# Performance work log

Measured on AMD Instinct MI355X. Metric: run time of the kernel, lower is better.

## Reference

```python
import jax, jax.numpy as jnp
import numpy as np

D = 128        # num_hidden
NIN = 384      # num_in (edge feature dim)
FF = 4 * D     # dense inner dim
SCALE = 30.0
EPS = 1e-5     # haiku LayerNorm default

gelu = lambda x: jax.nn.gelu(x, approximate=False)

def _ln(x, g, o):
    mu = jnp.mean(x, axis=-1, keepdims=True)
    var = jnp.var(x, axis=-1, keepdims=True)
    return (x - mu) * jax.lax.rsqrt(var + EPS) * g + o

def setup_inputs() -> dict:
    key = jax.random.key(0)
    ks = jax.random.split(key, 12)
    B, N, K = 4, 2048, 48
    s = lambda fan_in: 1.0 / np.sqrt(fan_in)
    return {
        "h_V": jax.random.normal(ks[0], (B, N, D), jnp.float32),
        "h_E": jax.random.normal(ks[1], (B, N, K, NIN), jnp.float32),
        "mask_V": jnp.ones((B, N), jnp.float32),
        "mask_attend": jnp.ones((B, N, K), jnp.float32),
        "W1": jax.random.normal(ks[2], (D + NIN, D), jnp.float32) * s(D + NIN),
        "b1": jnp.zeros((D,), jnp.float32),
        "W2": jax.random.normal(ks[3], (D, D), jnp.float32) * s(D),
        "b2": jnp.zeros((D,), jnp.float32),
        "W3": jax.random.normal(ks[4], (D, D), jnp.float32) * s(D),
        "b3": jnp.zeros((D,), jnp.float32),
        "W_in": jax.random.normal(ks[5], (D, FF), jnp.float32) * s(D),
        "b_in": jnp.zeros((FF,), jnp.float32),
        "W_out": jax.random.normal(ks[6], (FF, D), jnp.float32) * s(FF),
        "b_out": jnp.zeros((D,), jnp.float32),
        "g1": jnp.ones((D,), jnp.float32),
        "o1": jnp.zeros((D,), jnp.float32),
        "g2": jnp.ones((D,), jnp.float32),
        "o2": jnp.zeros((D,), jnp.float32),
    }

def reference(h_V, h_E, mask_V, mask_attend, W1, b1, W2, b2, W3, b3,
              W_in, b_in, W_out, b_out, g1, o1, g2, o2):
    B, N, K, _ = h_E.shape
    # broadcast node feats over neighbors and concat with edge feats: (B,N,K,D+NIN)
    h_V_exp = jnp.broadcast_to(h_V[:, :, None, :], (B, N, K, h_V.shape[-1]))
    h_EV = jnp.concatenate([h_V_exp, h_E], axis=-1)
    h = gelu(h_EV @ W1 + b1)
    h = gelu(h @ W2 + b2)
    h_message = h @ W3 + b3                      # (B,N,K,D)
    h_message = mask_attend[..., None] * h_message
    dh = jnp.sum(h_message, axis=-2) / SCALE      # (B,N,D)
    h_V = _ln(h_V + dh, g1, o1)                   # dropout rate=0 -> identity
    dh = gelu(h_V @ W_in + b_in) @ W_out + b_out  # position-wise FFN
    h_V = _ln(h_V + dh, g2, o2)
    h_V = mask_V[..., None] * h_V
    return h_V
```

## Files before the change

### kernel.cpp

```cpp
#include <hip/hip_runtime.h>
#include <hip/hip_bf16.h>

typedef unsigned short u16;
typedef __attribute__((ext_vector_type(8))) short short8;
typedef __attribute__((ext_vector_type(4))) float f32x4;

#define SD   128
#define SNIN 384
#define SK   48
#define HPAD 136
#define FPAD 520

#define OFF_W1A   0
#define OFF_W1B   32768
#define OFF_W2    131072
#define OFF_W3    163840
#define OFF_WIN   196608
#define OFF_WOUT  327680

__device__ __forceinline__ u16 f2b(float f){
  union { float f; unsigned u; } v; v.f = f;
  unsigned r = (v.u + 0x7FFFu + ((v.u >> 16) & 1u)) >> 16;
  return (u16)r;
}
__device__ __forceinline__ short8 ldg8(const u16* p){
  return *reinterpret_cast<const short8*>(p);
}
__device__ __forceinline__ short8 cvt8(const float* p){
  float4 a = *reinterpret_cast<const float4*>(p);
  float4 b = *reinterpret_cast<const float4*>(p + 4);
  short8 r;
  r[0]=(short)f2b(a.x); r[1]=(short)f2b(a.y); r[2]=(short)f2b(a.z); r[3]=(short)f2b(a.w);
  r[4]=(short)f2b(b.x); r[5]=(short)f2b(b.y); r[6]=(short)f2b(b.z); r[7]=(short)f2b(b.w);
  return r;
}

__device__ __forceinline__ float gelu_f(float x){
  float xc = fminf(3.0f, fmaxf(-3.0f, x));
  float u  = xc*xc;
  float p  = fmaf(u, fmaf(u, fmaf(u, -4.81034e-4f, 1.185750e-2f), -1.1877797e-1f), 7.9165011e-1f);
  float t  = xc*p;
  float hx = 0.5f*x;
  return fmaf(t, hx, hx);
}

__global__ __launch_bounds__(256) void prep_pack(
    const float* __restrict__ W1, const float* __restrict__ W2, const float* __restrict__ W3,
    const float* __restrict__ Win, const float* __restrict__ Wout, u16* __restrict__ ws)
{
  int t = blockIdx.x*256 + threadIdx.x;
  const float* src; int stride, rowoff, NT; u16* dst; int local;
  if (t < 2048)       { src=W1;  stride=SD;  rowoff=0;   NT=8;  dst=ws+OFF_W1A/2;  local=t;       }
  else if (t < 8192)  { src=W1;  stride=SD;  rowoff=128; NT=8;  dst=ws+OFF_W1B/2;  local=t-2048;  }
  else if (t < 10240) { src=W2;  stride=SD;  rowoff=0;   NT=8;  dst=ws+OFF_W2/2;   local=t-8192;  }
  else if (t < 12288) { src=W3;  stride=SD;  rowoff=0;   NT=8;  dst=ws+OFF_W3/2;   local=t-10240; }
  else if (t < 20480) { src=Win; stride=512; rowoff=0;   NT=32; dst=ws+OFF_WIN/2;  local=t-12288; }
  else                { src=Wout;stride=SD;  rowoff=0;   NT=8;  dst=ws+OFF_WOUT/2; local=t-20480; }
  int lane = local & 63;
  int blk  = local >> 6;
  int nt = blk % NT, ks = blk / NT;
  int k0 = rowoff + ks*32 + (lane>>4)*8;
  int n  = nt*16 + (lane & 15);
  union { u16 a[8]; short8 v; } tmp;
  #pragma unroll
  for (int j=0;j<8;j++) tmp.a[j] = f2b(src[(size_t)(k0+j)*stride + n]);
  *reinterpret_cast<short8*>(dst + (size_t)local*8) = tmp.v;
}

__global__ __launch_bounds__(256, 2) void dec_nodes(
    const float* __restrict__ hV, const float* __restrict__ hE, const float* __restrict__ mAtt,
    const float* __restrict__ b1, const float* __restrict__ b2, const float* __restrict__ b3,
    const float* __restrict__ g1, const float* __restrict__ o1,
    const u16* __restrict__ ws, float* __restrict__ u_out)
{
  __shared__ u16 HH[4][SK*HPAD];

  const int tid  = threadIdx.x;
  const int w    = tid >> 6;
  const int lane = tid & 63;
  const int quad = lane >> 4;
  const int l16  = lane & 15;
  const int g    = blockIdx.x*4 + w;
  u16* HHw = HH[w];

  float base1v[8];
  {
    f32x4 accb[8];
    #pragma unroll
    for (int nt=0;nt<8;nt++) accb[nt] = (f32x4){0.f,0.f,0.f,0.f};
    const u16* Bb = ws + OFF_W1A/2 + (size_t)lane*8;
    #pragma unroll
    for (int ks=0; ks<4; ks++){
      short8 af = cvt8(hV + (size_t)g*SD + ks*32 + quad*8);
      #pragma unroll
      for (int nt=0; nt<8; nt++){
        short8 bf = ldg8(Bb + ((size_t)(ks*8+nt)*64)*8);
        accb[nt] = __builtin_amdgcn_mfma_f32_16x16x32_bf16(af, bf, accb[nt], 0,0,0);
      }
    }
    #pragma unroll
    for (int nt=0;nt<8;nt++) base1v[nt] = accb[nt][0] + b1[nt*16 + l16];
  }

  f32x4 acc[24];
  #pragma unroll
  for (int i=0;i<24;i++) acc[i] = (f32x4){0.f,0.f,0.f,0.f};
  {
    const float* Ab = hE + (size_t)g*(SK*SNIN) + (size_t)l16*SNIN + quad*8;
    const u16*  Bb = ws + OFF_W1B/2 + (size_t)lane*8;
    #pragma unroll
    for (int ks=0; ks<12; ks++){
      short8 af[3];
      #pragma unroll
      for (int mt=0; mt<3; mt++) af[mt] = cvt8(Ab + (size_t)mt*16*SNIN + ks*32);
      #pragma unroll
      for (int nt=0; nt<8; nt++){
        short8 bf = ldg8(Bb + ((size_t)(ks*8+nt)*64)*8);
        #pragma unroll
        for (int mt=0; mt<3; mt++)
          acc[mt*8+nt] = __builtin_amdgcn_mfma_f32_16x16x32_bf16(af[mt], bf, acc[mt*8+nt], 0,0,0);
      }
    }
    #pragma unroll
    for (int mt=0; mt<3; mt++)
      #pragma unroll
      for (int nt=0; nt<8; nt++)
        #pragma unroll
        for (int i=0;i<4;i++){
          int row = mt*16 + quad*4 + i;
          HHw[row*HPAD + nt*16 + l16] = f2b(gelu_f(acc[mt*8+nt][i] + base1v[nt]));
        }
  }
  __syncthreads();

  #pragma unroll
  for (int i=0;i<24;i++) acc[i] = (f32x4){0.f,0.f,0.f,0.f};
  {
    const u16* Bb = ws + OFF_W2/2 + (size_t)lane*8;
    #pragma unroll
    for (int ks=0; ks<4; ks++){
      short8 af[3];
      #pragma unroll
      for (int mt=0; mt<3; mt++)
        af[mt] = *reinterpret_cast<const short8*>(&HHw[(mt*16+l16)*HPAD + ks*32 + quad*8]);
      #pragma unroll
      for (int nt=0; nt<8; nt++){
        short8 bf = ldg8(Bb + ((size_t)(ks*8+nt)*64)*8);
        #pragma unroll
        for (int mt=0; mt<3; mt++)
          acc[mt*8+nt] = __builtin_amdgcn_mfma_f32_16x16x32_bf16(af[mt], bf, acc[mt*8+nt], 0,0,0);
      }
    }
  }
  __syncthreads();
  {
    #pragma unroll
    for (int mt=0; mt<3; mt++)
      #pragma unroll
      for (int nt=0; nt<8; nt++){
        float bb = b2[nt*16 + l16];
        #pragma unroll
        for (int i=0;i<4;i++){
          int row = mt*16 + quad*4 + i;
          HHw[row*HPAD + nt*16 + l16] = f2b(gelu_f(acc[mt*8+nt][i] + bb));
        }
      }
  }
  __syncthreads();

  #pragma unroll
  for (int i=0;i<24;i++) acc[i] = (f32x4){0.f,0.f,0.f,0.f};
  {
    const u16* Bb = ws + OFF_W3/2 + (size_t)lane*8;
    #pragma unroll
    for (int ks=0; ks<4; ks++){
      short8 af[3];
      #pragma unroll
      for (int mt=0; mt<3; mt++)
        af[mt] = *reinterpret_cast<const short8*>(&HHw[(mt*16+l16)*HPAD + ks*32 + quad*8]);
      #pragma unroll
      for (int nt=0; nt<8; nt++){
        short8 bf = ldg8(Bb + ((size_t)(ks*8+nt)*64)*8);
        #pragma unroll
        for (int mt=0; mt<3; mt++)
          acc[mt*8+nt] = __builtin_amdgcn_mfma_f32_16x16x32_bf16(af[mt], bf, acc[mt*8+nt], 0,0,0);
      }
    }
  }
  float p[8];
  {
    #pragma unroll
    for (int nt=0;nt<8;nt++) p[nt] = 0.f;
    #pragma unroll
    for (int mt=0; mt<3; mt++)
      #pragma unroll
      for (int i=0;i<4;i++){
        float m = mAtt[(size_t)g*SK + mt*16 + quad*4 + i];
        #pragma unroll
        for (int nt=0; nt<8; nt++){
          float bb = b3[nt*16 + l16];
          p[nt] = fmaf(m, acc[mt*8+nt][i] + bb, p[nt]);
        }
      }
    #pragma unroll
    for (int nt=0;nt<8;nt++){
      p[nt] += __shfl_down(p[nt], 32, 64);
      p[nt] += __shfl_down(p[nt], 16, 64);
      p[nt]  = __shfl(p[nt], l16, 64);
    }
  }

  {
    float x[8];
    float s = 0.f, q = 0.f;
    #pragma unroll
    for (int nt=0;nt<8;nt++){
      x[nt] = hV[(size_t)g*SD + nt*16 + l16] + p[nt]*(1.0f/30.0f);
      s += x[nt]; q = fmaf(x[nt], x[nt], q);
    }
    #pragma unroll
    for (int off=1; off<64; off<<=1){ s += __shfl_xor(s, off, 64); q += __shfl_xor(q, off, 64); }
    float mu  = s * (1.0f/512.0f);
    float var = q * (1.0f/512.0f) - mu*mu;
    float rs  = rsqrtf(var + 1e-5f);
    #pragma unroll
    for (int k=0;k<2;k++){
      int nt = 2*quad + k;
      float uv = (x[nt]-mu)*rs*g1[nt*16+l16] + o1[nt*16+l16];
      u_out[(size_t)g*SD + nt*16 + l16] = uv;
    }
  }
}

__global__ __launch_bounds__(128) void ffn_ln(
    const float* __restrict__ b_in, const float* __restrict__ b_out,
    const float* __restrict__ g2, const float* __restrict__ o2, const float* __restrict__ mV,
    const u16* __restrict__ ws, float* __restrict__ uo)
{
  __shared__ u16 fS[2][16*FPAD];
  const int tid = threadIdx.x, w = tid>>6, lane = tid&63, quad = lane>>4, l16 = lane&15;
  const int m0 = blockIdx.x*32 + w*16;

  short8 afr[4];
  const float* Ap = uo + (size_t)(m0 + l16)*SD + quad*8;
  #pragma unroll
  for (int ks=0; ks<4; ks++) afr[ks] = cvt8(Ap + ks*32);

  #pragma unroll
  for (int nb=0; nb<4; nb++){
    f32x4 acc[8];
    #pragma unroll
    for (int t=0;t<8;t++) acc[t] = (f32x4){0.f,0.f,0.f,0.f};
    const u16* Bp = ws + OFF_WIN/2 + ((size_t)(nb*8)*64 + lane)*8;
    #pragma unroll
    for (int ks=0; ks<4; ks++){
      #pragma unroll
      for (int t=0;t<8;t++){
        short8 bf = ldg8(Bp + ((size_t)ks*32 + t)*512);
        acc[t] = __builtin_amdgcn_mfma_f32_16x16x32_bf16(afr[ks], bf, acc[t], 0,0,0);
      }
    }
    #pragma unroll
    for (int t=0;t<8;t++){
      int coln = nb*128 + t*16 + l16;
      float bi = b_in[coln];
      #pragma unroll
      for (int i=0;i<4;i++)
        fS[w][(quad*4+i)*FPAD + coln] = f2b(gelu_f(acc[t][i] + bi));
    }
  }
  __syncthreads();

  f32x4 acc2[8];
  #pragma unroll
  for (int t=0;t<8;t++) acc2[t] = (f32x4){0.f,0.f,0.f,0.f};
  const u16* Bo = ws + OFF_WOUT/2 + (size_t)lane*8;
  #pragma unroll
  for (int ks=0; ks<16; ks++){
    const short8 af = *reinterpret_cast<const short8*>(&fS[w][l16*FPAD + ks*32 + quad*8]);
    #pragma unroll
    for (int t=0;t<8;t++){
      short8 bf = ldg8(Bo + ((size_t)ks*8 + t)*512);
      acc2[t] = __builtin_amdgcn_mfma_f32_16x16x32_bf16(af, bf, acc2[t], 0,0,0);
    }
  }

  float bov[8], g2v[8], o2v[8];
  #pragma unroll
  for (int t=0;t<8;t++){
    int cl = t*16 + l16;
    bov[t] = b_out[cl]; g2v[t] = g2[cl]; o2v[t] = o2[cl];
  }
  #pragma unroll
  for (int i=0;i<4;i++){
    int r = m0 + quad*4 + i;
    float xv[8];
    float s = 0.f, q = 0.f;
    #pragma unroll
    for (int t=0;t<8;t++){
      xv[t] = uo[(size_t)r*SD + t*16 + l16] + acc2[t][i] + bov[t];
      s += xv[t]; q = fmaf(xv[t], xv[t], q);
    }
    #pragma unroll
    for (int mk=1; mk<16; mk<<=1){ s += __shfl_xor(s, mk, 64); q += __shfl_xor(q, mk, 64); }
    float mu  = s * (1.0f/128.0f);
    float var = q * (1.0f/128.0f) - mu*mu;
    float rs  = rsqrtf(var + 1e-5f);
    float mv  = mV[r];
    #pragma unroll
    for (int t=0;t<8;t++)
      uo[(size_t)r*SD + t*16 + l16] = mv * ((xv[t]-mu)*rs*g2v[t] + o2v[t]);
  }
}

extern "C" void kernel_launch(void* const* d_in, const int* in_sizes, int n_in,
                              void* d_out, int out_size, void* d_ws, size_t ws_size,
                              hipStream_t stream) {
  (void)n_in; (void)out_size; (void)ws_size;
  const float* hV    = (const float*)d_in[0];
  const float* hE    = (const float*)d_in[1];
  const float* mV    = (const float*)d_in[2];
  const float* mAtt  = (const float*)d_in[3];
  const float* W1    = (const float*)d_in[4];
  const float* b1    = (const float*)d_in[5];
  const float* W2    = (const float*)d_in[6];
  const float* b2    = (const float*)d_in[7];
  const float* W3    = (const float*)d_in[8];
  const float* b3    = (const float*)d_in[9];
  const float* Win   = (const float*)d_in[10];
  const float* b_in  = (const float*)d_in[11];
  const float* Wout  = (const float*)d_in[12];
  const float* b_out = (const float*)d_in[13];
  const float* g1    = (const float*)d_in[14];
  const float* o1    = (const float*)d_in[15];
  const float* g2    = (const float*)d_in[16];
  const float* o2    = (const float*)d_in[17];
  u16*   ws   = (u16*)d_ws;
  float* outp = (float*)d_out;
  const int NG = in_sizes[0] / SD;

  hipLaunchKernelGGL(prep_pack, dim3(112), dim3(256), 0, stream, W1, W2, W3, Win, Wout, ws);
  hipLaunchKernelGGL(dec_nodes, dim3(NG/4), dim3(256), 0, stream,
                     hV, hE, mAtt, b1, b2, b3, g1, o1, ws, outp);
  hipLaunchKernelGGL(ffn_ln, dim3(NG/32), dim3(128), 0, stream,
                     b_in, b_out, g2, o2, mV, ws, outp);
}
```

Before: 1.005 ms.

## Prefetch hE and weight fragments, use hardware bf16 pack, re-split FFN across waves

Replaces the software bf16 rounding with v_cvt_pk_bf16_f32 inline asm. It software-pipelines the first edge GEMM by loading hE tiles two k-steps ahead in rotating register buffers, and double-buffers weight fragments in the 128x128 GEMMs. The FFN kernel is restructured so four waves share 16 rows, splitting the hidden and output columns across waves and staging through shared memory. The aim is to hide global load latency on the hE stream and raise FFN parallelism, at the cost of more registers, which could cut occupancy under the (256,2) launch bounds.

```diff
diff --git a/kernel.cpp b/kernel.cpp
--- a/kernel.cpp
+++ b/kernel.cpp
@@ -26,13 +26,18 @@
 __device__ __forceinline__ short8 ldg8(const u16* p){
   return *reinterpret_cast<const short8*>(p);
 }
+__device__ __forceinline__ short8 pack8(float4 a, float4 b){
+  union { unsigned u[4]; short8 s; } r;
+  asm("v_cvt_pk_bf16_f32 %0, %1, %2" : "=v"(r.u[0]) : "v"(a.x), "v"(a.y));
+  asm("v_cvt_pk_bf16_f32 %0, %1, %2" : "=v"(r.u[1]) : "v"(a.z), "v"(a.w));
+  asm("v_cvt_pk_bf16_f32 %0, %1, %2" : "=v"(r.u[2]) : "v"(b.x), "v"(b.y));
+  asm("v_cvt_pk_bf16_f32 %0, %1, %2" : "=v"(r.u[3]) : "v"(b.z), "v"(b.w));
+  return r.s;
+}
 __device__ __forceinline__ short8 cvt8(const float* p){
   float4 a = *reinterpret_cast<const float4*>(p);
   float4 b = *reinterpret_cast<const float4*>(p + 4);
-  short8 r;
-  r[0]=(short)f2b(a.x); r[1]=(short)f2b(a.y); r[2]=(short)f2b(a.z); r[3]=(short)f2b(a.w);
-  r[4]=(short)f2b(b.x); r[5]=(short)f2b(b.y); r[6]=(short)f2b(b.z); r[7]=(short)f2b(b.w);
-  return r;
+  return pack8(a, b);
 }
 
 __device__ __forceinline__ float gelu_f(float x){
@@ -67,6 +72,55 @@
   *reinterpret_cast<short8*>(dst + (size_t)local*8) = tmp.v;
 }
 
+__device__ __forceinline__ void mlp128(const u16* __restrict__ Bb, const u16* HHw,
+                                       int l16, int quad, f32x4 acc[24])
+{
+  short8 bc[8], bn[8];
+  #pragma unroll
+  for (int nt=0;nt<8;nt++) bc[nt] = ldg8(Bb + ((size_t)nt*64)*8);
+  #pragma unroll
+  for (int ks=0; ks<4; ks++){
+    if (ks < 3){
+      #pragma unroll
+      for (int nt=0;nt<8;nt++) bn[nt] = ldg8(Bb + ((size_t)((ks+1)*8+nt)*64)*8);
+    }
+    short8 af[3];
+    #pragma unroll
+    for (int mt=0; mt<3; mt++)
+      af[mt] = *reinterpret_cast<const short8*>(&HHw[(size_t)(mt*16+l16)*HPAD + ks*32 + quad*8]);
+    #pragma unroll
+    for (int nt=0; nt<8; nt++)
+      #pragma unroll
+      for (int mt=0; mt<3; mt++)
+        acc[mt*8+nt] = __builtin_amdgcn_mfma_f32_16x16x32_bf16(af[mt], bc[nt], acc[mt*8+nt], 0,0,0);
+    if (ks < 3){
+      #pragma unroll
+      for (int nt=0;nt<8;nt++) bc[nt] = bn[nt];
+    }
+  }
+}
+
+#define LDA(BUF, kk) { _Pragma("unroll") for (int mt=0; mt<3; mt++){ \
+    BUF[mt][0] = *reinterpret_cast<const float4*>(Ab + (size_t)mt*16*SNIN + (kk)*32); \
+    BUF[mt][1] = *reinterpret_cast<const float4*>(Ab + (size_t)mt*16*SNIN + (kk)*32 + 4); } }
+
+#define G1STEP(CUR, NXT, ks, PF) { \
+    if (PF) LDA(NXT, (ks)+2); \
+    short8 af[3]; \
+    _Pragma("unroll") for (int mt=0; mt<3; mt++) af[mt] = pack8(CUR[mt][0], CUR[mt][1]); \
+    _Pragma("unroll") for (int nt=0; nt<8; nt++){ \
+      short8 bf = ldg8(Bb + ((size_t)((ks)*8+nt)*64)*8); \
+      _Pragma("unroll") for (int mt=0; mt<3; mt++) \
+        acc[mt*8+nt] = __builtin_amdgcn_mfma_f32_16x16x32_bf16(af[mt], bf, acc[mt*8+nt], 0,0,0); \
+    } }
+
+#define B1STEP(HB, ks) { \
+    short8 af = pack8(HB[0], HB[1]); \
+    _Pragma("unroll") for (int nt=0; nt<8; nt++){ \
+      short8 bf = ldg8(Bb1 + ((size_t)((ks)*8+nt)*64)*8); \
+      accb[nt] = __builtin_amdgcn_mfma_f32_16x16x32_bf16(af, bf, accb[nt], 0,0,0); \
+    } }
+
 __global__ __launch_bounds__(256, 2) void dec_nodes(
     const float* __restrict__ hV, const float* __restrict__ hE, const float* __restrict__ mAtt,
     const float* __restrict__ b1, const float* __restrict__ b2, const float* __restrict__ b3,
@@ -88,16 +142,14 @@
     f32x4 accb[8];
     #pragma unroll
     for (int nt=0;nt<8;nt++) accb[nt] = (f32x4){0.f,0.f,0.f,0.f};
-    const u16* Bb = ws + OFF_W1A/2 + (size_t)lane*8;
-    #pragma unroll
-    for (int ks=0; ks<4; ks++){
-      short8 af = cvt8(hV + (size_t)g*SD + ks*32 + quad*8);
-      #pragma unroll
-      for (int nt=0; nt<8; nt++){
-        short8 bf = ldg8(Bb + ((size_t)(ks*8+nt)*64)*8);
-        accb[nt] = __builtin_amdgcn_mfma_f32_16x16x32_bf16(af, bf, accb[nt], 0,0,0);
-      }
-    }
+    const u16* Bb1 = ws + OFF_W1A/2 + (size_t)lane*8;
+    const float* hp = hV + (size_t)g*SD + quad*8;
+    float4 H0[2], H1[2], H2[2], H3[2];
+    H0[0] = *reinterpret_cast<const float4*>(hp);       H0[1] = *reinterpret_cast<const float4*>(hp+4);
+    H1[0] = *reinterpret_cast<const float4*>(hp+32);    H1[1] = *reinterpret_cast<const float4*>(hp+36);
+    H2[0] = *reinterpret_cast<const float4*>(hp+64);    H2[1] = *reinterpret_cast<const float4*>(hp+68);
+    H3[0] = *reinterpret_cast<const float4*>(hp+96);    H3[1] = *reinterpret_cast<const float4*>(hp+100);
+    B1STEP(H0,0); B1STEP(H1,1); B1STEP(H2,2); B1STEP(H3,3);
     #pragma unroll
     for (int nt=0;nt<8;nt++) base1v[nt] = accb[nt][0] + b1[nt*16 + l16];
   }
@@ -108,19 +160,12 @@
   {
     const float* Ab = hE + (size_t)g*(SK*SNIN) + (size_t)l16*SNIN + quad*8;
     const u16*  Bb = ws + OFF_W1B/2 + (size_t)lane*8;
-    #pragma unroll
-    for (int ks=0; ks<12; ks++){
-      short8 af[3];
-      #pragma unroll
-      for (int mt=0; mt<3; mt++) af[mt] = cvt8(Ab + (size_t)mt*16*SNIN + ks*32);
-      #pragma unroll
-      for (int nt=0; nt<8; nt++){
-        short8 bf = ldg8(Bb + ((size_t)(ks*8+nt)*64)*8);
-        #pragma unroll
-        for (int mt=0; mt<3; mt++)
-          acc[mt*8+nt] = __builtin_amdgcn_mfma_f32_16x16x32_bf16(af[mt], bf, acc[mt*8+nt], 0,0,0);
-      }
-    }
+    float4 A0[3][2], A1[3][2], A2[3][2];
+    LDA(A0,0); LDA(A1,1);
+    G1STEP(A0,A2,0,1);  G1STEP(A1,A0,1,1);  G1STEP(A2,A1,2,1);
+    G1STEP(A0,A2,3,1);  G1STEP(A1,A0,4,1);  G1STEP(A2,A1,5,1);
+    G1STEP(A0,A2,6,1);  G1STEP(A1,A0,7,1);  G1STEP(A2,A1,8,1);
+    G1STEP(A0,A2,9,1);  G1STEP(A1,A0,10,0); G1STEP(A2,A1,11,0);
     #pragma unroll
     for (int mt=0; mt<3; mt++)
       #pragma unroll
@@ -135,23 +180,7 @@
 
   #pragma unroll
   for (int i=0;i<24;i++) acc[i] = (f32x4){0.f,0.f,0.f,0.f};
-  {
-    const u16* Bb = ws + OFF_W2/2 + (size_t)lane*8;
-    #pragma unroll
-    for (int ks=0; ks<4; ks++){
-      short8 af[3];
-      #pragma unroll
-      for (int mt=0; mt<3; mt++)
-        af[mt] = *reinterpret_cast<const short8*>(&HHw[(mt*16+l16)*HPAD + ks*32 + quad*8]);
-      #pragma unroll
-      for (int nt=0; nt<8; nt++){
-        short8 bf = ldg8(Bb + ((size_t)(ks*8+nt)*64)*8);
-        #pragma unroll
-        for (int mt=0; mt<3; mt++)
-          acc[mt*8+nt] = __builtin_amdgcn_mfma_f32_16x16x32_bf16(af[mt], bf, acc[mt*8+nt], 0,0,0);
-      }
-    }
-  }
+  mlp128(ws + OFF_W2/2 + (size_t)lane*8, HHw, l16, quad, acc);
   __syncthreads();
   {
     #pragma unroll
@@ -170,23 +199,7 @@
 
   #pragma unroll
   for (int i=0;i<24;i++) acc[i] = (f32x4){0.f,0.f,0.f,0.f};
-  {
-    const u16* Bb = ws + OFF_W3/2 + (size_t)lane*8;
-    #pragma unroll
-    for (int ks=0; ks<4; ks++){
-      short8 af[3];
-      #pragma unroll
-      for (int mt=0; mt<3; mt++)
-        af[mt] = *reinterpret_cast<const short8*>(&HHw[(mt*16+l16)*HPAD + ks*32 + quad*8]);
-      #pragma unroll
-      for (int nt=0; nt<8; nt++){
-        short8 bf = ldg8(Bb + ((size_t)(ks*8+nt)*64)*8);
-        #pragma unroll
-        for (int mt=0; mt<3; mt++)
-          acc[mt*8+nt] = __builtin_amdgcn_mfma_f32_16x16x32_bf16(af[mt], bf, acc[mt*8+nt], 0,0,0);
-      }
-    }
-  }
+  mlp128(ws + OFF_W3/2 + (size_t)lane*8, HHw, l16, quad, acc);
   float p[8];
   {
     #pragma unroll
@@ -232,26 +245,26 @@
   }
 }
 
-__global__ __launch_bounds__(128) void ffn_ln(
+__global__ __launch_bounds__(256) void ffn_ln(
     const float* __restrict__ b_in, const float* __restrict__ b_out,
     const float* __restrict__ g2, const float* __restrict__ o2, const float* __restrict__ mV,
     const u16* __restrict__ ws, float* __restrict__ uo)
 {
-  __shared__ u16 fS[2][16*FPAD];
+  __shared__ u16 fS[16*FPAD];
+  __shared__ float dS[16][132];
   const int tid = threadIdx.x, w = tid>>6, lane = tid&63, quad = lane>>4, l16 = lane&15;
-  const int m0 = blockIdx.x*32 + w*16;
+  const int m0 = blockIdx.x*16;
 
   short8 afr[4];
   const float* Ap = uo + (size_t)(m0 + l16)*SD + quad*8;
   #pragma unroll
   for (int ks=0; ks<4; ks++) afr[ks] = cvt8(Ap + ks*32);
 
-  #pragma unroll
-  for (int nb=0; nb<4; nb++){
+  {
     f32x4 acc[8];
     #pragma unroll
     for (int t=0;t<8;t++) acc[t] = (f32x4){0.f,0.f,0.f,0.f};
-    const u16* Bp = ws + OFF_WIN/2 + ((size_t)(nb*8)*64 + lane)*8;
+    const u16* Bp = ws + OFF_WIN/2 + ((size_t)(w*8)*64 + lane)*8;
     #pragma unroll
     for (int ks=0; ks<4; ks++){
       #pragma unroll
@@ -262,43 +275,47 @@
     }
     #pragma unroll
     for (int t=0;t<8;t++){
-      int coln = nb*128 + t*16 + l16;
+      int coln = w*128 + t*16 + l16;
       float bi = b_in[coln];
       #pragma unroll
       for (int i=0;i<4;i++)
-        fS[w][(quad*4+i)*FPAD + coln] = f2b(gelu_f(acc[t][i] + bi));
-    }
-  }
-  __syncthreads();
-
-  f32x4 acc2[8];
-  #pragma unroll
-  for (int t=0;t<8;t++) acc2[t] = (f32x4){0.f,0.f,0.f,0.f};
-  const u16* Bo = ws + OFF_WOUT/2 + (size_t)lane*8;
-  #pragma unroll
-  for (int ks=0; ks<16; ks++){
-    const short8 af = *reinterpret_cast<const short8*>(&fS[w][l16*FPAD + ks*32 + quad*8]);
+        fS[(quad*4+i)*FPAD + coln] = f2b(gelu_f(acc[t][i] + bi));
+    }
+  }
+  __syncthreads();
+
+  {
+    f32x4 acc2[2];
+    acc2[0] = (f32x4){0.f,0.f,0.f,0.f};
+    acc2[1] = (f32x4){0.f,0.f,0.f,0.f};
+    const u16* Bo = ws + OFF_WOUT/2 + (size_t)lane*8;
+    #pragma unroll
+    for (int ks=0; ks<16; ks++){
+      const short8 af = *reinterpret_cast<const short8*>(&fS[l16*FPAD + ks*32 + quad*8]);
+      #pragma unroll
+      for (int j=0;j<2;j++){
+        short8 bf = ldg8(Bo + ((size_t)ks*8 + (w*2+j))*512);
+        acc2[j] = __builtin_amdgcn_mfma_f32_16x16x32_bf16(af, bf, acc2[j], 0,0,0);
+      }
+    }
+    #pragma unroll
+    for (int j=0;j<2;j++){
+      int cl = (w*2+j)*16 + l16;
+      float bo = b_out[cl];
+      #pragma unroll
+      for (int i=0;i<4;i++)
+        dS[quad*4+i][cl] = acc2[j][i] + bo;
+    }
+  }
+  __syncthreads();
+
+  {
+    int rl = w*4 + quad;
+    int r  = m0 + rl;
+    float xv[8]; float s = 0.f, q = 0.f;
     #pragma unroll
     for (int t=0;t<8;t++){
-      short8 bf = ldg8(Bo + ((size_t)ks*8 + t)*512);
-      acc2[t] = __builtin_amdgcn_mfma_f32_16x16x32_bf16(af, bf, acc2[t], 0,0,0);
-    }
-  }
-
-  float bov[8], g2v[8], o2v[8];
-  #pragma unroll
-  for (int t=0;t<8;t++){
-    int cl = t*16 + l16;
-    bov[t] = b_out[cl]; g2v[t] = g2[cl]; o2v[t] = o2[cl];
-  }
-  #pragma unroll
-  for (int i=0;i<4;i++){
-    int r = m0 + quad*4 + i;
-    float xv[8];
-    float s = 0.f, q = 0.f;
-    #pragma unroll
-    for (int t=0;t<8;t++){
-      xv[t] = uo[(size_t)r*SD + t*16 + l16] + acc2[t][i] + bov[t];
+      xv[t] = uo[(size_t)r*SD + t*16 + l16] + dS[rl][t*16 + l16];
       s += xv[t]; q = fmaf(xv[t], xv[t], q);
     }
     #pragma unroll
@@ -308,8 +325,10 @@
     float rs  = rsqrtf(var + 1e-5f);
     float mv  = mV[r];
     #pragma unroll
-    for (int t=0;t<8;t++)
-      uo[(size_t)r*SD + t*16 + l16] = mv * ((xv[t]-mu)*rs*g2v[t] + o2v[t]);
+    for (int t=0;t<8;t++){
+      int cl = t*16 + l16;
+      uo[(size_t)r*SD + cl] = mv * ((xv[t]-mu)*rs*g2[cl] + o2[cl]);
+    }
   }
 }
 
@@ -342,6 +361,6 @@
   hipLaunchKernelGGL(prep_pack, dim3(112), dim3(256), 0, stream, W1, W2, W3, Win, Wout, ws);
   hipLaunchKernelGGL(dec_nodes, dim3(NG/4), dim3(256), 0, stream,
                      hV, hE, mAtt, b1, b2, b3, g1, o1, ws, outp);
-  hipLaunchKernelGGL(ffn_ln, dim3(NG/32), dim3(128), 0, stream,
+  hipLaunchKernelGGL(ffn_ln, dim3(NG/16), dim3(256), 0, stream,
                      b_in, b_out, g2, o2, mV, ws, outp);
 }
```

Result: faster. 904.5 us (-10.0%).
